# Kernel tuning notes

Measured on AMD Instinct MI355X. Metric: run time of the kernel, lower is better.

## Reference

```python
import jax, jax.numpy as jnp
import numpy as np

B, D, H, O = 8192, 1024, 4096, 1024
E, S = 8, 2  # routed experts, shared experts


def setup_inputs() -> dict:
    key = jax.random.key(0)
    ks = jax.random.split(key, 12)
    sd = lambda n: 1.0 / np.sqrt(n)
    return {
        "x": jax.random.normal(ks[0], (B, D), jnp.float32),
        "W1": jax.random.normal(ks[1], (E, D, H), jnp.float32) * sd(D),
        "b1": jnp.zeros((E, H), jnp.float32),
        "W2": jax.random.normal(ks[2], (E, H, O), jnp.float32) * sd(H),
        "b2": jnp.zeros((E, O), jnp.float32),
        "Ws1": jax.random.normal(ks[3], (S, D, H), jnp.float32) * sd(D),
        "bs1": jnp.zeros((S, H), jnp.float32),
        "Ws2": jax.random.normal(ks[4], (S, H, O), jnp.float32) * sd(H),
        "bs2": jnp.zeros((S, O), jnp.float32),
        "Wg": jax.random.normal(ks[5], (D, E + S), jnp.float32) * sd(D),
        "bg": jnp.zeros((E + S,), jnp.float32),
        "k": 2,
    }


def _expert_mlp(x, W1, b1, W2, b2):
    # x: [B,D], W1: [n,D,H] -> [B,n,O]; dropout is identity in eval mode
    h = jax.nn.relu(jnp.einsum("bd,ndh->bnh", x, W1) + b1[None])
    return jnp.einsum("bnh,nho->bno", h, W2) + b2[None]


def reference(x, W1, b1, W2, b2, Ws1, bs1, Ws2, bs2, Wg, bg, k):
    gate_scores = jax.nn.softmax(x @ Wg + bg, axis=-1)        # [B, S+E]
    shared_gate = gate_scores[:, :S]                          # [B, S]
    expert_gate = gate_scores[:, S:]                          # [B, E]

    expert_outputs = _expert_mlp(x, W1, b1, W2, b2)           # [B, E, O]
    shared_outputs = _expert_mlp(x, Ws1, bs1, Ws2, bs2)       # [B, S, O]
    shared_output = jnp.einsum("bs,bso->bo", shared_gate, shared_outputs)

    # sparse top-k combine (vectorized equivalent of the per-sample loop)
    topk_score, topk_idx = jax.lax.top_k(expert_gate, k)      # [B, k]
    gathered = jnp.take_along_axis(expert_outputs, topk_idx[:, :, None], axis=1)  # [B,k,O]
    output = jnp.einsum("bk,bko->bo", topk_score, gathered) + shared_output
    return output
```

## Files before the change

### kernel.cpp

```cpp
#include <hip/hip_runtime.h>
#include <stdint.h>

#define Bn 8192
#define Dn 1024
#define Hn 4096
#define On 1024
#define En 8
#define Sn 2

typedef __attribute__((ext_vector_type(8))) short short8;
typedef __attribute__((ext_vector_type(4))) float f32x4;
typedef __attribute__((ext_vector_type(16))) float f32x16;

__device__ __forceinline__ unsigned short f2bf(float f) {
  unsigned int u = __float_as_uint(f);
  u += 0x7fff + ((u >> 16) & 1);
  return (unsigned short)(u >> 16);
}

__device__ __forceinline__ void gload16(const void* g, void* l) {
  __builtin_amdgcn_global_load_lds(
      (const __attribute__((address_space(1))) unsigned int*)g,
      (__attribute__((address_space(3))) unsigned int*)l, 16, 0, 0);
}

__global__ __launch_bounds__(256) void gate_k(
    const float* __restrict__ x, const float* __restrict__ Wg,
    const float* __restrict__ bg, unsigned short* __restrict__ xb,
    float* __restrict__ rw, int* __restrict__ ri) {
  {
    size_t base = (size_t)blockIdx.x * 1024;
    const float4* xi = (const float4*)x + base;
    ushort4* xo = (ushort4*)xb + base;
#pragma unroll
    for (int k2 = 0; k2 < 4; k2++) {
      float4 v = xi[k2 * 256 + threadIdx.x];
      ushort4 o;
      o.x = f2bf(v.x); o.y = f2bf(v.y); o.z = f2bf(v.z); o.w = f2bf(v.w);
      xo[k2 * 256 + threadIdx.x] = o;
    }
  }
  __shared__ __align__(16) float wgs[Dn * 10];
  for (int i = threadIdx.x; i < 2560; i += 256)
    ((float4*)wgs)[i] = ((const float4*)Wg)[i];
  __syncthreads();
  int lane = threadIdx.x & 63, wave = threadIdx.x >> 6;
  int r = blockIdx.x * 4 + wave;
  const float* xr = x + (size_t)r * Dn;
  float p[10];
#pragma unroll
  for (int j = 0; j < 10; j++) p[j] = 0.f;
  for (int d = lane; d < Dn; d += 64) {
    float xv = xr[d];
#pragma unroll
    for (int j = 0; j < 10; j++) p[j] += xv * wgs[d * 10 + j];
  }
#pragma unroll
  for (int off = 32; off; off >>= 1)
#pragma unroll
    for (int j = 0; j < 10; j++) p[j] += __shfl_xor(p[j], off);
  float mx = -1e30f;
#pragma unroll
  for (int j = 0; j < 10; j++) { p[j] += bg[j]; mx = fmaxf(mx, p[j]); }
  float s = 0.f;
#pragma unroll
  for (int j = 0; j < 10; j++) { p[j] = expf(p[j] - mx); s += p[j]; }
  float inv = 1.f / s;
  int i0 = 2, i1 = 2; float v0 = -1e30f, v1 = -1e30f;
#pragma unroll
  for (int j = 2; j < 10; j++) {
    float v = p[j];
    if (v > v0) { v1 = v0; i1 = i0; v0 = v; i0 = j; }
    else if (v > v1) { v1 = v; i1 = j; }
  }
  if (lane == 0) {
    rw[r * 4 + 0] = v0 * inv;
    rw[r * 4 + 1] = v1 * inv;
    rw[r * 4 + 2] = p[0] * inv;
    rw[r * 4 + 3] = p[1] * inv;
    ri[r * 2 + 0] = i0 - 2;
    ri[r * 2 + 1] = i1 - 2;
  }
}

__global__ __launch_bounds__(256) void count_k(const int* __restrict__ ri,
                                               int* __restrict__ cnt) {
  int c[8];
#pragma unroll
  for (int j = 0; j < 8; j++) c[j] = 0;
  int base = blockIdx.x * 1024;
  for (int i = threadIdx.x; i < 1024; i += 256) {
    int e = ri[base + i];
#pragma unroll
    for (int j = 0; j < 8; j++) c[j] += (e == j) ? 1 : 0;
  }
#pragma unroll
  for (int j = 0; j < 8; j++)
#pragma unroll
    for (int off = 32; off; off >>= 1) c[j] += __shfl_xor(c[j], off);
  __shared__ int sc[4][8];
  int wv = threadIdx.x >> 6, lane = threadIdx.x & 63;
  if (lane == 0)
#pragma unroll
    for (int j = 0; j < 8; j++) sc[wv][j] = c[j];
  __syncthreads();
  if (threadIdx.x < 8)
    atomicAdd(&cnt[threadIdx.x], sc[0][threadIdx.x] + sc[1][threadIdx.x] +
                                 sc[2][threadIdx.x] + sc[3][threadIdx.x]);
}

__global__ __launch_bounds__(256) void tcvt_all(
    const float* __restrict__ W1, const float* __restrict__ W2,
    const float* __restrict__ Ws1, const float* __restrict__ Ws2,
    unsigned short* __restrict__ w1t, unsigned short* __restrict__ w2t,
    unsigned short* __restrict__ ws1t, unsigned short* __restrict__ ws2t) {
  __shared__ float t[128][65];
  int bid = blockIdx.x;
  int u = bid >> 9, r = bid & 511;
  const float* in; unsigned short* out; int Kd, Nd;
  if (u < 8)       { Kd = Dn; Nd = Hn; in = W1  + (size_t)u * Dn * Hn;        out = w1t  + (size_t)u * Dn * Hn; }
  else if (u < 16) { Kd = Hn; Nd = On; in = W2  + (size_t)(u - 8) * Hn * On;  out = w2t  + (size_t)(u - 8) * Hn * On; }
  else if (u < 18) { Kd = Dn; Nd = Hn; in = Ws1 + (size_t)(u - 16) * Dn * Hn; out = ws1t + (size_t)(u - 16) * Dn * Hn; }
  else             { Kd = Hn; Nd = On; in = Ws2 + (size_t)(u - 18) * Hn * On; out = ws2t + (size_t)(u - 18) * Hn * On; }
  int by, bx;
  if (Kd == Dn) { by = (r & 7) * 128;  bx = (r >> 3) * 64; }
  else          { by = (r & 31) * 128; bx = (r >> 5) * 64; }
  int tid = threadIdx.x;
#pragma unroll
  for (int q = 0; q < 8; q++) {
    int idx = q * 256 + tid;
    int k = idx >> 4, f4 = (idx & 15) * 4;
    float4 v = *(const float4*)&in[(size_t)(by + k) * Nd + bx + f4];
    t[k][f4] = v.x; t[k][f4 + 1] = v.y; t[k][f4 + 2] = v.z; t[k][f4 + 3] = v.w;
  }
  __syncthreads();
  int KC = Kd >> 3;
#pragma unroll
  for (int p = 0; p < 4; p++) {
    int idx = p * 256 + tid;
    int nl = idx & 63, kgi = idx >> 6;
    int kg = kgi * 8;
    int ng = bx + nl;
    short8 v;
#pragma unroll
    for (int j = 0; j < 8; j++) v[j] = (short)f2bf(t[kg + j][nl]);
    size_t o = ((((size_t)(ng >> 8) * KC + (by >> 3) + kgi) * 256 + (ng & 255)) << 3);
    *(short8*)&out[o] = v;
  }
}

__global__ __launch_bounds__(256) void build_k(
    const float* __restrict__ rw, const int* __restrict__ ri,
    const int* __restrict__ cnt, int* __restrict__ cnt2,
    int* __restrict__ slot_row, float* __restrict__ slot_w,
    int* __restrict__ slot_dst) {
  __shared__ int lcnt[8], lbase[8];
  int tid = threadIdx.x;
  if (tid < 8) lcnt[tid] = 0;
  __syncthreads();
  int r = blockIdx.x * 256 + tid;
  int e0 = ri[r * 2 + 0], e1 = ri[r * 2 + 1];
  int rk0 = atomicAdd(&lcnt[e0], 1);
  int rk1 = atomicAdd(&lcnt[e1], 1);
  __syncthreads();
  if (tid < 8) lbase[tid] = atomicAdd(&cnt2[tid], lcnt[tid]);
  __syncthreads();
  int off0 = 0, off1 = 0;
#pragma unroll
  for (int i = 0; i < 8; i++) {
    int ci = cnt[i];
    off0 += (i < e0) ? ci : 0;
    off1 += (i < e1) ? ci : 0;
  }
  int s0 = off0 + lbase[e0] + rk0;
  int s1 = off1 + lbase[e1] + rk1;
  slot_row[s0] = r; slot_w[s0] = rw[r * 4 + 0]; slot_dst[s0] = r * 4 + 0;
  slot_row[s1] = r; slot_w[s1] = rw[r * 4 + 1]; slot_dst[s1] = r * 4 + 1;
#pragma unroll
  for (int s = 0; s < 2; s++) {
    int slot = 16384 + s * Bn + r;
    slot_row[slot] = r;
    slot_w[slot] = rw[r * 4 + 2 + s];
    slot_dst[slot] = r * 4 + 2 + s;
  }
}


__global__ __launch_bounds__(512, 4) void gemm1_u(
    const unsigned short* __restrict__ xb,
    const unsigned short* __restrict__ w1c, const unsigned short* __restrict__ ws1c,
    const float* __restrict__ b1, const float* __restrict__ bs1,
    const int* __restrict__ cnt, const int* __restrict__ slotRow,
    unsigned short* __restrict__ h, int ubase, int hsh) {
  int total = gridDim.x;
  int gid = blockIdx.x;
  int swz = (gid & 7) * (total >> 3) + (gid >> 3);
  int u = ubase + (swz >> 10);
  int rem = swz & 1023;
  int mt = rem & 63;
  int nt = rem >> 6;

  int M, off, hoff;
  const unsigned short* Bte; const float* be;
  if (u < 8) {
    M = cnt[u]; off = 0;
    for (int i = 0; i < u; i++) off += cnt[i];
    hoff = off;
    Bte = w1c + (size_t)u * Hn * Dn; be = b1 + (size_t)u * Hn;
  } else {
    int s = u - 8;
    M = Bn; off = 16384 + s * Bn; hoff = hsh + s * Bn;
    Bte = ws1c + (size_t)s * Hn * Dn; be = bs1 + (size_t)s * Hn;
  }
  int mbase = mt * 128;
  if (mbase >= M) return;
  int n0 = nt * 256;

  __shared__ __align__(16) unsigned short shb[36864];

  int tid = threadIdx.x;
  int lane = tid & 63, wv = tid >> 6;
  int wm = wv >> 2, wn = wv & 3;
  int l31 = lane & 31, l5 = lane >> 5;
  int rswA = (l31 >> 1) & 3;

  int scol = (((tid & 3) ^ ((tid >> 3) & 3)) * 8);
  int mi = mbase + (tid >> 2);
  if (mi > M - 1) mi = M - 1;
  int grow = slotRow[off + mi];
  const unsigned short* agp = xb + (size_t)grow * Dn + scol;
  const unsigned short* Bnt = Bte + (size_t)nt * 262144;
  const unsigned short* bgp0 = Bnt + (((size_t)(tid >> 8) * 256 + (tid & 255)) << 3);
  const unsigned short* bgp1 = bgp0 + 4096;

  f32x16 acc[2][2];
#pragma unroll
  for (int i = 0; i < 2; i++)
#pragma unroll
    for (int j = 0; j < 2; j++)
#pragma unroll
      for (int q = 0; q < 16; q++) acc[i][j][q] = 0.f;

  auto STAGE = [&](int slot, int tt) {
    int so = slot * 12288;
    gload16(agp + tt * 32, &shb[so + wv * 512]);
    gload16(bgp0 + tt * 8192, &shb[so + 4096 + wv * 512]);
    gload16(bgp1 + tt * 8192, &shb[so + 8192 + wv * 512]);
  };
  auto COMPUTE = [&](int slot) {
    int so = slot * 12288;
#pragma unroll
    for (int kk = 0; kk < 2; kk++) {
      int cA = (((kk * 2 + l5) ^ rswA) * 8);
      short8 a0 = *(const short8*)&shb[so + (wm * 64 + l31) * 32 + cA];
      short8 a1 = *(const short8*)&shb[so + (wm * 64 + 32 + l31) * 32 + cA];
      int cB = (kk * 2 + l5) * 256;
      short8 b0 = *(const short8*)&shb[so + 4096 + (cB + wn * 64 + l31) * 8];
      short8 b1 = *(const short8*)&shb[so + 4096 + (cB + wn * 64 + 32 + l31) * 8];
      acc[0][0] = __builtin_amdgcn_mfma_f32_32x32x16_bf16(a0, b0, acc[0][0], 0, 0, 0);
      acc[0][1] = __builtin_amdgcn_mfma_f32_32x32x16_bf16(a0, b1, acc[0][1], 0, 0, 0);
      acc[1][0] = __builtin_amdgcn_mfma_f32_32x32x16_bf16(a1, b0, acc[1][0], 0, 0, 0);
      acc[1][1] = __builtin_amdgcn_mfma_f32_32x32x16_bf16(a1, b1, acc[1][1], 0, 0, 0);
    }
  };

  const int NT = Dn >> 5;
  int sA = 0, sB = 1, sC = 2;
  STAGE(0, 0);
  STAGE(1, 1);
  for (int t = 0; t < NT; ++t) {
    int tn = (t + 2 < NT) ? (t + 2) : (NT - 1);
    STAGE(sC, tn);
    asm volatile("s_waitcnt vmcnt(6)" ::: "memory");
    asm volatile("s_barrier" ::: "memory");
    COMPUTE(sA);
    asm volatile("s_barrier" ::: "memory");
    int tmp = sA; sA = sB; sB = sC; sC = tmp;
  }

  float bev[2];
#pragma unroll
  for (int g = 0; g < 2; g++) bev[g] = be[n0 + wn * 64 + g * 32 + l31];
#pragma unroll
  for (int i = 0; i < 2; i++) {
#pragma unroll
    for (int reg = 0; reg < 16; reg++) {
      int rr = (reg & 3) + 8 * (reg >> 2) + 4 * l5;
      int m = mbase + wm * 64 + i * 32 + rr;
      if (m < M) {
        size_t hrow = (size_t)(hoff + m) * Hn;
#pragma unroll
        for (int g = 0; g < 2; g++) {
          int n = n0 + wn * 64 + g * 32 + l31;
          float v = acc[i][g][reg] + bev[g];
          h[hrow + n] = f2bf(fmaxf(v, 0.f));
        }
      }
    }
  }
}

__global__ __launch_bounds__(512, 4) void gemm2_u(
    const unsigned short* __restrict__ hin,
    const unsigned short* __restrict__ w2c, const unsigned short* __restrict__ ws2c,
    const float* __restrict__ b2, const float* __restrict__ bs2,
    const int* __restrict__ cnt, const float* __restrict__ slotW,
    const int* __restrict__ slotDst, float* __restrict__ Y, int ubase, int hsh) {
  int total = gridDim.x;
  int gid = blockIdx.x;
  int swz = (gid & 7) * (total >> 3) + (gid >> 3);
  int u = ubase + (swz >> 8);
  int rem = swz & 255;
  int mt = rem & 63;
  int nt = rem >> 6;

  int M, off, hoff;
  const unsigned short* Bte; const float* be;
  if (u < 8) {
    M = cnt[u]; off = 0;
    for (int i = 0; i < u; i++) off += cnt[i];
    hoff = off;
    Bte = w2c + (size_t)u * On * Hn; be = b2 + (size_t)u * On;
  } else {
    int s = u - 8;
    M = Bn; off = 16384 + s * Bn; hoff = hsh + s * Bn;
    Bte = ws2c + (size_t)s * On * Hn; be = bs2 + (size_t)s * On;
  }
  int mbase = mt * 128;
  if (mbase >= M) return;
  int n0 = nt * 256;

  __shared__ __align__(16) unsigned short shb[36864];

  int tid = threadIdx.x;
  int lane = tid & 63, wv = tid >> 6;
  int wm = wv >> 2, wn = wv & 3;
  int l31 = lane & 31, l5 = lane >> 5;
  int rswA = (l31 >> 1) & 3;

  int scol = (((tid & 3) ^ ((tid >> 3) & 3)) * 8);
  int mi = mbase + (tid >> 2);
  if (mi > M - 1) mi = M - 1;
  const unsigned short* agp = hin + (size_t)(hoff + mi) * Hn + scol;
  const unsigned short* Bnt = Bte + (size_t)nt * 1048576;
  const unsigned short* bgp0 = Bnt + (((size_t)(tid >> 8) * 256 + (tid & 255)) << 3);
  const unsigned short* bgp1 = bgp0 + 4096;

  f32x16 acc[2][2];
#pragma unroll
  for (int i = 0; i < 2; i++)
#pragma unroll
    for (int j = 0; j < 2; j++)
#pragma unroll
      for (int q = 0; q < 16; q++) acc[i][j][q] = 0.f;

  auto STAGE = [&](int slot, int tt) {
    int so = slot * 12288;
    gload16(agp + tt * 32, &shb[so + wv * 512]);
    gload16(bgp0 + tt * 8192, &shb[so + 4096 + wv * 512]);
    gload16(bgp1 + tt * 8192, &shb[so + 8192 + wv * 512]);
  };
  auto COMPUTE = [&](int slot) {
    int so = slot * 12288;
#pragma unroll
    for (int kk = 0; kk < 2; kk++) {
      int cA = (((kk * 2 + l5) ^ rswA) * 8);
      short8 a0 = *(const short8*)&shb[so + (wm * 64 + l31) * 32 + cA];
      short8 a1 = *(const short8*)&shb[so + (wm * 64 + 32 + l31) * 32 + cA];
      int cB = (kk * 2 + l5) * 256;
      short8 b0 = *(const short8*)&shb[so + 4096 + (cB + wn * 64 + l31) * 8];
      short8 b1 = *(const short8*)&shb[so + 4096 + (cB + wn * 64 + 32 + l31) * 8];
      acc[0][0] = __builtin_amdgcn_mfma_f32_32x32x16_bf16(a0, b0, acc[0][0], 0, 0, 0);
      acc[0][1] = __builtin_amdgcn_mfma_f32_32x32x16_bf16(a0, b1, acc[0][1], 0, 0, 0);
      acc[1][0] = __builtin_amdgcn_mfma_f32_32x32x16_bf16(a1, b0, acc[1][0], 0, 0, 0);
      acc[1][1] = __builtin_amdgcn_mfma_f32_32x32x16_bf16(a1, b1, acc[1][1], 0, 0, 0);
    }
  };

  const int NT = Hn >> 5;
  int sA = 0, sB = 1, sC = 2;
  STAGE(0, 0);
  STAGE(1, 1);
  for (int t = 0; t < NT; ++t) {
    int tn = (t + 2 < NT) ? (t + 2) : (NT - 1);
    STAGE(sC, tn);
    asm volatile("s_waitcnt vmcnt(6)" ::: "memory");
    asm volatile("s_barrier" ::: "memory");
    COMPUTE(sA);
    asm volatile("s_barrier" ::: "memory");
    int tmp = sA; sA = sB; sB = sC; sC = tmp;
  }

  float bev[2];
#pragma unroll
  for (int g = 0; g < 2; g++) bev[g] = be[n0 + wn * 64 + g * 32 + l31];
#pragma unroll
  for (int i = 0; i < 2; i++) {
#pragma unroll
    for (int reg = 0; reg < 16; reg++) {
      int rr = (reg & 3) + 8 * (reg >> 2) + 4 * l5;
      int m = mbase + wm * 64 + i * 32 + rr;
      if (m < M) {
        float wgt = slotW[off + m];
        size_t yrow = (size_t)slotDst[off + m] * On;
#pragma unroll
        for (int g = 0; g < 2; g++) {
          int n = n0 + wn * 64 + g * 32 + l31;
          Y[yrow + n] = wgt * (acc[i][g][reg] + bev[g]);
        }
      }
    }
  }
}

__global__ void final_k(const float* __restrict__ Y, float* __restrict__ out) {
  int i = blockIdx.x * 256 + threadIdx.x;
  int b = i >> 8;
  int c = i & 255;
  const float4* y = (const float4*)Y;
  float4 a0 = y[((size_t)b * 4 + 0) * 256 + c];
  float4 a1 = y[((size_t)b * 4 + 1) * 256 + c];
  float4 a2 = y[((size_t)b * 4 + 2) * 256 + c];
  float4 a3 = y[((size_t)b * 4 + 3) * 256 + c];
  float4 o;
  o.x = a0.x + a1.x + a2.x + a3.x;
  o.y = a0.y + a1.y + a2.y + a3.y;
  o.z = a0.z + a1.z + a2.z + a3.z;
  o.w = a0.w + a1.w + a2.w + a3.w;
  ((float4*)out)[i] = o;
}

extern "C" void kernel_launch(void* const* d_in, const int* in_sizes, int n_in,
                              void* d_out, int out_size, void* d_ws, size_t ws_size,
                              hipStream_t stream) {
  const float* x   = (const float*)d_in[0];
  const float* W1  = (const float*)d_in[1];
  const float* b1  = (const float*)d_in[2];
  const float* W2  = (const float*)d_in[3];
  const float* b2  = (const float*)d_in[4];
  const float* Ws1 = (const float*)d_in[5];
  const float* bs1 = (const float*)d_in[6];
  const float* Ws2 = (const float*)d_in[7];
  const float* bs2 = (const float*)d_in[8];
  const float* Wg  = (const float*)d_in[9];
  const float* bg  = (const float*)d_in[10];
  float* out = (float*)d_out;

  auto plan = [&](int hrows, size_t* need,
                  unsigned short** xb, unsigned short** w1t, unsigned short** w2t,
                  unsigned short** ws1t, unsigned short** ws2t, unsigned short** hbuf,
                  float** Y, float** rw, int** ri, int** ctrl,
                  int** slot_row, float** slot_w, int** slot_dst) {
    char* w = (char*)d_ws;
    size_t p = 0;
    auto alloc = [&](size_t n) { char* r = w + p; p = (p + n + 255) & ~(size_t)255; return r; };
    *xb   = (unsigned short*)alloc((size_t)Bn * Dn * 2);
    *w1t  = (unsigned short*)alloc((size_t)En * Hn * Dn * 2);
    *w2t  = (unsigned short*)alloc((size_t)En * On * Hn * 2);
    *ws1t = (unsigned short*)alloc((size_t)Sn * Hn * Dn * 2);
    *ws2t = (unsigned short*)alloc((size_t)Sn * On * Hn * 2);
    *hbuf = (unsigned short*)alloc((size_t)hrows * Hn * 2);
    *Y    = (float*)alloc((size_t)Bn * 4 * On * 4);
    *rw   = (float*)alloc((size_t)Bn * 4 * 4);
    *ri   = (int*)alloc((size_t)Bn * 2 * 4);
    *ctrl = (int*)alloc(256);
    *slot_row = (int*)alloc((size_t)32768 * 4);
    *slot_w   = (float*)alloc((size_t)32768 * 4);
    *slot_dst = (int*)alloc((size_t)32768 * 4);
    *need = p;
  };

  unsigned short *xb, *w1t, *w2t, *ws1t, *ws2t, *hbuf;
  float *Y, *rw, *slot_w;
  int *ri, *ctrl, *slot_row, *slot_dst;
  size_t need;
  plan(32768, &need, &xb, &w1t, &w2t, &ws1t, &ws2t, &hbuf, &Y, &rw, &ri, &ctrl,
       &slot_row, &slot_w, &slot_dst);
  int big = (need <= ws_size);
  if (!big) {
    plan(16384, &need, &xb, &w1t, &w2t, &ws1t, &ws2t, &hbuf, &Y, &rw, &ri, &ctrl,
         &slot_row, &slot_w, &slot_dst);
    if (need > ws_size) return;
  }

  int* cnt  = ctrl;
  int* cnt2 = ctrl + 8;

  hipMemsetAsync(ctrl, 0, 64, stream);
  gate_k<<<2048, 256, 0, stream>>>(x, Wg, bg, xb, rw, ri);
  tcvt_all<<<10240, 256, 0, stream>>>(W1, W2, Ws1, Ws2, w1t, w2t, ws1t, ws2t);
  count_k<<<16, 256, 0, stream>>>(ri, cnt);
  build_k<<<32, 256, 0, stream>>>(rw, ri, cnt, cnt2, slot_row, slot_w, slot_dst);

  if (big) {
    gemm1_u<<<10 * 1024, 512, 0, stream>>>(xb, w1t, ws1t, b1, bs1, cnt, slot_row,
                                           hbuf, 0, 16384);
    gemm2_u<<<10 * 256, 512, 0, stream>>>(hbuf, w2t, ws2t, b2, bs2, cnt, slot_w,
                                          slot_dst, Y, 0, 16384);
  } else {
    gemm1_u<<<8 * 1024, 512, 0, stream>>>(xb, w1t, ws1t, b1, bs1, cnt, slot_row,
                                          hbuf, 0, 0);
    gemm2_u<<<8 * 256, 512, 0, stream>>>(hbuf, w2t, ws2t, b2, bs2, cnt, slot_w,
                                         slot_dst, Y, 0, 0);
    gemm1_u<<<2 * 1024, 512, 0, stream>>>(xb, w1t, ws1t, b1, bs1, cnt, slot_row,
                                          hbuf, 8, 0);
    gemm2_u<<<2 * 256, 512, 0, stream>>>(hbuf, w2t, ws2t, b2, bs2, cnt, slot_w,
                                         slot_dst, Y, 8, 0);
  }
  final_k<<<8192, 256, 0, stream>>>(Y, out);
}
```

Baseline: 849.6 us.

## Interleave LDS fragment loads with MFMA and fuse combine via atomics

```diff
diff --git a/kernel.cpp b/kernel.cpp
--- a/kernel.cpp
+++ b/kernel.cpp
@@ -241,39 +241,54 @@
 #pragma unroll
       for (int q = 0; q < 16; q++) acc[i][j][q] = 0.f;
 
-  auto STAGE = [&](int slot, int tt) {
-    int so = slot * 12288;
-    gload16(agp + tt * 32, &shb[so + wv * 512]);
-    gload16(bgp0 + tt * 8192, &shb[so + 4096 + wv * 512]);
-    gload16(bgp1 + tt * 8192, &shb[so + 8192 + wv * 512]);
-  };
-  auto COMPUTE = [&](int slot) {
-    int so = slot * 12288;
-#pragma unroll
-    for (int kk = 0; kk < 2; kk++) {
-      int cA = (((kk * 2 + l5) ^ rswA) * 8);
-      short8 a0 = *(const short8*)&shb[so + (wm * 64 + l31) * 32 + cA];
-      short8 a1 = *(const short8*)&shb[so + (wm * 64 + 32 + l31) * 32 + cA];
-      int cB = (kk * 2 + l5) * 256;
-      short8 b0 = *(const short8*)&shb[so + 4096 + (cB + wn * 64 + l31) * 8];
-      short8 b1 = *(const short8*)&shb[so + 4096 + (cB + wn * 64 + 32 + l31) * 8];
-      acc[0][0] = __builtin_amdgcn_mfma_f32_32x32x16_bf16(a0, b0, acc[0][0], 0, 0, 0);
-      acc[0][1] = __builtin_amdgcn_mfma_f32_32x32x16_bf16(a0, b1, acc[0][1], 0, 0, 0);
-      acc[1][0] = __builtin_amdgcn_mfma_f32_32x32x16_bf16(a1, b0, acc[1][0], 0, 0, 0);
-      acc[1][1] = __builtin_amdgcn_mfma_f32_32x32x16_bf16(a1, b1, acc[1][1], 0, 0, 0);
-    }
+  auto FRAG = [&](int so, int kk, short8& a0, short8& a1, short8& b0, short8& b1) {
+    int cA = (((kk * 2 + l5) ^ rswA) * 8);
+    a0 = *(const short8*)&shb[so + (wm * 64 + l31) * 32 + cA];
+    a1 = *(const short8*)&shb[so + (wm * 64 + 32 + l31) * 32 + cA];
+    int cB = (kk * 2 + l5) * 256;
+    b0 = *(const short8*)&shb[so + 4096 + (cB + wn * 64 + l31) * 8];
+    b1 = *(const short8*)&shb[so + 4096 + (cB + wn * 64 + 32 + l31) * 8];
   };
 
   const int NT = Dn >> 5;
   int sA = 0, sB = 1, sC = 2;
-  STAGE(0, 0);
-  STAGE(1, 1);
+  gload16(agp, &shb[wv * 512]);
+  gload16(bgp0, &shb[4096 + wv * 512]);
+  gload16(bgp1, &shb[8192 + wv * 512]);
+  gload16(agp + 32, &shb[12288 + wv * 512]);
+  gload16(bgp0 + 8192, &shb[12288 + 4096 + wv * 512]);
+  gload16(bgp1 + 8192, &shb[12288 + 8192 + wv * 512]);
+  asm volatile("s_waitcnt vmcnt(3)" ::: "memory");
+  asm volatile("s_barrier" ::: "memory");
   for (int t = 0; t < NT; ++t) {
     int tn = (t + 2 < NT) ? (t + 2) : (NT - 1);
-    STAGE(sC, tn);
-    asm volatile("s_waitcnt vmcnt(6)" ::: "memory");
-    asm volatile("s_barrier" ::: "memory");
-    COMPUTE(sA);
+    int soA = sA * 12288, soC = sC * 12288;
+    short8 a0, a1, b0, b1;
+    FRAG(soA, 0, a0, a1, b0, b1);
+    gload16(agp + tn * 32, &shb[soC + wv * 512]);
+    gload16(bgp0 + tn * 8192, &shb[soC + 4096 + wv * 512]);
+    asm volatile("s_barrier" ::: "memory");
+    asm volatile("s_waitcnt lgkmcnt(0)" ::: "memory");
+    __builtin_amdgcn_sched_barrier(0);
+    __builtin_amdgcn_s_setprio(1);
+    acc[0][0] = __builtin_amdgcn_mfma_f32_32x32x16_bf16(a0, b0, acc[0][0], 0, 0, 0);
+    acc[0][1] = __builtin_amdgcn_mfma_f32_32x32x16_bf16(a0, b1, acc[0][1], 0, 0, 0);
+    acc[1][0] = __builtin_amdgcn_mfma_f32_32x32x16_bf16(a1, b0, acc[1][0], 0, 0, 0);
+    acc[1][1] = __builtin_amdgcn_mfma_f32_32x32x16_bf16(a1, b1, acc[1][1], 0, 0, 0);
+    __builtin_amdgcn_s_setprio(0);
+    asm volatile("s_barrier" ::: "memory");
+    FRAG(soA, 1, a0, a1, b0, b1);
+    gload16(bgp1 + tn * 8192, &shb[soC + 8192 + wv * 512]);
+    asm volatile("s_waitcnt vmcnt(3)" ::: "memory");
+    asm volatile("s_barrier" ::: "memory");
+    asm volatile("s_waitcnt lgkmcnt(0)" ::: "memory");
+    __builtin_amdgcn_sched_barrier(0);
+    __builtin_amdgcn_s_setprio(1);
+    acc[0][0] = __builtin_amdgcn_mfma_f32_32x32x16_bf16(a0, b0, acc[0][0], 0, 0, 0);
+    acc[0][1] = __builtin_amdgcn_mfma_f32_32x32x16_bf16(a0, b1, acc[0][1], 0, 0, 0);
+    acc[1][0] = __builtin_amdgcn_mfma_f32_32x32x16_bf16(a1, b0, acc[1][0], 0, 0, 0);
+    acc[1][1] = __builtin_amdgcn_mfma_f32_32x32x16_bf16(a1, b1, acc[1][1], 0, 0, 0);
+    __builtin_amdgcn_s_setprio(0);
     asm volatile("s_barrier" ::: "memory");
     int tmp = sA; sA = sB; sB = sC; sC = tmp;
   }
@@ -305,7 +320,7 @@
     const unsigned short* __restrict__ w2c, const unsigned short* __restrict__ ws2c,
     const float* __restrict__ b2, const float* __restrict__ bs2,
     const int* __restrict__ cnt, const float* __restrict__ slotW,
-    const int* __restrict__ slotDst, float* __restrict__ Y, int ubase, int hsh) {
+    const int* __restrict__ slotDst, float* __restrict__ outp, int ubase, int hsh) {
   int total = gridDim.x;
   int gid = blockIdx.x;
   int swz = (gid & 7) * (total >> 3) + (gid >> 3);
@@ -354,39 +369,54 @@
 #pragma unroll
       for (int q = 0; q < 16; q++) acc[i][j][q] = 0.f;
 
-  auto STAGE = [&](int slot, int tt) {
-    int so = slot * 12288;
-    gload16(agp + tt * 32, &shb[so + wv * 512]);
-    gload16(bgp0 + tt * 8192, &shb[so + 4096 + wv * 512]);
-    gload16(bgp1 + tt * 8192, &shb[so + 8192 + wv * 512]);
-  };
-  auto COMPUTE = [&](int slot) {
-    int so = slot * 12288;
-#pragma unroll
-    for (int kk = 0; kk < 2; kk++) {
-      int cA = (((kk * 2 + l5) ^ rswA) * 8);
-      short8 a0 = *(const short8*)&shb[so + (wm * 64 + l31) * 32 + cA];
-      short8 a1 = *(const short8*)&shb[so + (wm * 64 + 32 + l31) * 32 + cA];
-      int cB = (kk * 2 + l5) * 256;
-      short8 b0 = *(const short8*)&shb[so + 4096 + (cB + wn * 64 + l31) * 8];
-      short8 b1 = *(const short8*)&shb[so + 4096 + (cB + wn * 64 + 32 + l31) * 8];
-      acc[0][0] = __builtin_amdgcn_mfma_f32_32x32x16_bf16(a0, b0, acc[0][0], 0, 0, 0);
-      acc[0][1] = __builtin_amdgcn_mfma_f32_32x32x16_bf16(a0, b1, acc[0][1], 0, 0, 0);
-      acc[1][0] = __builtin_amdgcn_mfma_f32_32x32x16_bf16(a1, b0, acc[1][0], 0, 0, 0);
-      acc[1][1] = __builtin_amdgcn_mfma_f32_32x32x16_bf16(a1, b1, acc[1][1], 0, 0, 0);
-    }
+  auto FRAG = [&](int so, int kk, short8& a0, short8& a1, short8& b0, short8& b1) {
+    int cA = (((kk * 2 + l5) ^ rswA) * 8);
+    a0 = *(const short8*)&shb[so + (wm * 64 + l31) * 32 + cA];
+    a1 = *(const short8*)&shb[so + (wm * 64 + 32 + l31) * 32 + cA];
+    int cB = (kk * 2 + l5) * 256;
+    b0 = *(const short8*)&shb[so + 4096 + (cB + wn * 64 + l31) * 8];
+    b1 = *(const short8*)&shb[so + 4096 + (cB + wn * 64 + 32 + l31) * 8];
   };
 
   const int NT = Hn >> 5;
   int sA = 0, sB = 1, sC = 2;
-  STAGE(0, 0);
-  STAGE(1, 1);
+  gload16(agp, &shb[wv * 512]);
+  gload16(bgp0, &shb[4096 + wv * 512]);
+  gload16(bgp1, &shb[8192 + wv * 512]);
+  gload16(agp + 32, &shb[12288 + wv * 512]);
+  gload16(bgp0 + 8192, &shb[12288 + 4096 + wv * 512]);
+  gload16(bgp1 + 8192, &shb[12288 + 8192 + wv * 512]);
+  asm volatile("s_waitcnt vmcnt(3)" ::: "memory");
+  asm volatile("s_barrier" ::: "memory");
   for (int t = 0; t < NT; ++t) {
     int tn = (t + 2 < NT) ? (t + 2) : (NT - 1);
-    STAGE(sC, tn);
-    asm volatile("s_waitcnt vmcnt(6)" ::: "memory");
-    asm volatile("s_barrier" ::: "memory");
-    COMPUTE(sA);
+    int soA = sA * 12288, soC = sC * 12288;
+    short8 a0, a1, b0, b1;
+    FRAG(soA, 0, a0, a1, b0, b1);
+    gload16(agp + tn * 32, &shb[soC + wv * 512]);
+    gload16(bgp0 + tn * 8192, &shb[soC + 4096 + wv * 512]);
+    asm volatile("s_barrier" ::: "memory");
+    asm volatile("s_waitcnt lgkmcnt(0)" ::: "memory");
+    __builtin_amdgcn_sched_barrier(0);
+    __builtin_amdgcn_s_setprio(1);
+    acc[0][0] = __builtin_amdgcn_mfma_f32_32x32x16_bf16(a0, b0, acc[0][0], 0, 0, 0);
+    acc[0][1] = __builtin_amdgcn_mfma_f32_32x32x16_bf16(a0, b1, acc[0][1], 0, 0, 0);
+    acc[1][0] = __builtin_amdgcn_mfma_f32_32x32x16_bf16(a1, b0, acc[1][0], 0, 0, 0);
+    acc[1][1] = __builtin_amdgcn_mfma_f32_32x32x16_bf16(a1, b1, acc[1][1], 0, 0, 0);
+    __builtin_amdgcn_s_setprio(0);
+    asm volatile("s_barrier" ::: "memory");
+    FRAG(soA, 1, a0, a1, b0, b1);
+    gload16(bgp1 + tn * 8192, &shb[soC + 8192 + wv * 512]);
+    asm volatile("s_waitcnt vmcnt(3)" ::: "memory");
+    asm volatile("s_barrier" ::: "memory");
+    asm volatile("s_waitcnt lgkmcnt(0)" ::: "memory");
+    __builtin_amdgcn_sched_barrier(0);
+    __builtin_amdgcn_s_setprio(1);
+    acc[0][0] = __builtin_amdgcn_mfma_f32_32x32x16_bf16(a0, b0, acc[0][0], 0, 0, 0);
+    acc[0][1] = __builtin_amdgcn_mfma_f32_32x32x16_bf16(a0, b1, acc[0][1], 0, 0, 0);
+    acc[1][0] = __builtin_amdgcn_mfma_f32_32x32x16_bf16(a1, b0, acc[1][0], 0, 0, 0);
+    acc[1][1] = __builtin_amdgcn_mfma_f32_32x32x16_bf16(a1, b1, acc[1][1], 0, 0, 0);
+    __builtin_amdgcn_s_setprio(0);
     asm volatile("s_barrier" ::: "memory");
     int tmp = sA; sA = sB; sB = sC; sC = tmp;
   }
@@ -402,32 +432,15 @@
       int m = mbase + wm * 64 + i * 32 + rr;
       if (m < M) {
         float wgt = slotW[off + m];
-        size_t yrow = (size_t)slotDst[off + m] * On;
+        size_t orow = (size_t)(slotDst[off + m] >> 2) * On;
 #pragma unroll
         for (int g = 0; g < 2; g++) {
           int n = n0 + wn * 64 + g * 32 + l31;
-          Y[yrow + n] = wgt * (acc[i][g][reg] + bev[g]);
+          atomicAdd(&outp[orow + n], wgt * (acc[i][g][reg] + bev[g]));
         }
       }
     }
   }
-}
-
-__global__ void final_k(const float* __restrict__ Y, float* __restrict__ out) {
-  int i = blockIdx.x * 256 + threadIdx.x;
-  int b = i >> 8;
-  int c = i & 255;
-  const float4* y = (const float4*)Y;
-  float4 a0 = y[((size_t)b * 4 + 0) * 256 + c];
-  float4 a1 = y[((size_t)b * 4 + 1) * 256 + c];
-  float4 a2 = y[((size_t)b * 4 + 2) * 256 + c];
-  float4 a3 = y[((size_t)b * 4 + 3) * 256 + c];
-  float4 o;
-  o.x = a0.x + a1.x + a2.x + a3.x;
-  o.y = a0.y + a1.y + a2.y + a3.y;
-  o.z = a0.z + a1.z + a2.z + a3.z;
-  o.w = a0.w + a1.w + a2.w + a3.w;
-  ((float4*)out)[i] = o;
 }
 
 extern "C" void kernel_launch(void* const* d_in, const int* in_sizes, int n_in,
@@ -449,7 +462,7 @@
   auto plan = [&](int hrows, size_t* need,
                   unsigned short** xb, unsigned short** w1t, unsigned short** w2t,
                   unsigned short** ws1t, unsigned short** ws2t, unsigned short** hbuf,
-                  float** Y, float** rw, int** ri, int** ctrl,
+                  float** rw, int** ri, int** ctrl,
                   int** slot_row, float** slot_w, int** slot_dst) {
     char* w = (char*)d_ws;
     size_t p = 0;
@@ -460,7 +473,6 @@
     *ws1t = (unsigned short*)alloc((size_t)Sn * Hn * Dn * 2);
     *ws2t = (unsigned short*)alloc((size_t)Sn * On * Hn * 2);
     *hbuf = (unsigned short*)alloc((size_t)hrows * Hn * 2);
-    *Y    = (float*)alloc((size_t)Bn * 4 * On * 4);
     *rw   = (float*)alloc((size_t)Bn * 4 * 4);
     *ri   = (int*)alloc((size_t)Bn * 2 * 4);
     *ctrl = (int*)alloc(256);
@@ -471,14 +483,14 @@
   };
 
   unsigned short *xb, *w1t, *w2t, *ws1t, *ws2t, *hbuf;
-  float *Y, *rw, *slot_w;
+  float *rw, *slot_w;
   int *ri, *ctrl, *slot_row, *slot_dst;
   size_t need;
-  plan(32768, &need, &xb, &w1t, &w2t, &ws1t, &ws2t, &hbuf, &Y, &rw, &ri, &ctrl,
+  plan(32768, &need, &xb, &w1t, &w2t, &ws1t, &ws2t, &hbuf, &rw, &ri, &ctrl,
        &slot_row, &slot_w, &slot_dst);
   int big = (need <= ws_size);
   if (!big) {
-    plan(16384, &need, &xb, &w1t, &w2t, &ws1t, &ws2t, &hbuf, &Y, &rw, &ri, &ctrl,
+    plan(16384, &need, &xb, &w1t, &w2t, &ws1t, &ws2t, &hbuf, &rw, &ri, &ctrl,
          &slot_row, &slot_w, &slot_dst);
     if (need > ws_size) return;
   }
@@ -487,6 +499,7 @@
   int* cnt2 = ctrl + 8;
 
   hipMemsetAsync(ctrl, 0, 64, stream);
+  hipMemsetAsync(out, 0, (size_t)Bn * On * sizeof(float), stream);
   gate_k<<<2048, 256, 0, stream>>>(x, Wg, bg, xb, rw, ri);
   tcvt_all<<<10240, 256, 0, stream>>>(W1, W2, Ws1, Ws2, w1t, w2t, ws1t, ws2t);
   count_k<<<16, 256, 0, stream>>>(ri, cnt);
@@ -496,16 +509,15 @@
     gemm1_u<<<10 * 1024, 512, 0, stream>>>(xb, w1t, ws1t, b1, bs1, cnt, slot_row,
                                            hbuf, 0, 16384);
     gemm2_u<<<10 * 256, 512, 0, stream>>>(hbuf, w2t, ws2t, b2, bs2, cnt, slot_w,
-                                          slot_dst, Y, 0, 16384);
+                                          slot_dst, out, 0, 16384);
   } else {
     gemm1_u<<<8 * 1024, 512, 0, stream>>>(xb, w1t, ws1t, b1, bs1, cnt, slot_row,
                                           hbuf, 0, 0);
     gemm2_u<<<8 * 256, 512, 0, stream>>>(hbuf, w2t, ws2t, b2, bs2, cnt, slot_w,
-                                         slot_dst, Y, 0, 0);
+                                         slot_dst, out, 0, 0);
     gemm1_u<<<2 * 1024, 512, 0, stream>>>(xb, w1t, ws1t, b1, bs1, cnt, slot_row,
                                           hbuf, 8, 0);
     gemm2_u<<<2 * 256, 512, 0, stream>>>(hbuf, w2t, ws2t, b2, bs2, cnt, slot_w,
-                                         slot_dst, Y, 8, 0);
-  }
-  final_k<<<8192, 256, 0, stream>>>(Y, out);
-}
+                                         slot_dst, out, 8, 0);
+  }
+}
```

Result: slower. 1.495 ms (+75.9%).
